# Performance work log

Measured on AMD Instinct MI355X. Metric: run time of the kernel, lower is better.

Reference implementation:

```python
import jax, jax.numpy as jnp
import numpy as np
from jax import lax

D_MODEL = 640
D_INNER = 1280
D_STATE = 34
D_CONV = 4
DT_RANK = 40  # ceil(640/16)
DT_MIN, DT_MAX = 1e-3, 1e-1
NUM_LAYERS = 8
BATCH, SEQ = 2, 2048


def setup_inputs() -> dict:
    key = jax.random.key(0)
    ks = jax.random.split(key, 8)
    hidden_states = jax.random.normal(ks[0], (BATCH, SEQ, D_MODEL), dtype=jnp.float32)
    W_in = jax.random.normal(ks[1], (2 * D_INNER, D_MODEL), dtype=jnp.float32) * 0.02
    conv_w = jax.random.normal(ks[2], (D_INNER, D_CONV), dtype=jnp.float32) * 0.2
    conv_b = jnp.zeros((D_INNER,), dtype=jnp.float32)
    W_x = jax.random.normal(ks[3], (DT_RANK + 2 * D_STATE, D_INNER), dtype=jnp.float32) * 0.02
    W_dt = jax.random.normal(ks[4], (D_INNER, DT_RANK), dtype=jnp.float32) * 0.02
    # dt bias init: inverse-softplus of dt sampled log-uniform in [dt_min, dt_max]
    u = jax.random.uniform(ks[5], (D_INNER,), dtype=jnp.float32)
    dt_vals = jnp.exp(u * (np.log(DT_MAX) - np.log(DT_MIN)) + np.log(DT_MIN))
    dt_bias = dt_vals + jnp.log(-jnp.expm1(-dt_vals))
    A_log = jnp.log(jnp.tile(jnp.arange(1, D_STATE + 1, dtype=jnp.float32)[None, :], (D_INNER, 1)))
    D_skip = jnp.ones((D_INNER,), dtype=jnp.float32)
    W_out = jax.random.normal(ks[6], (D_MODEL, D_INNER), dtype=jnp.float32) * (0.02 / np.sqrt(2.0 * NUM_LAYERS))
    return {"hidden_states": hidden_states, "W_in": W_in, "conv_w": conv_w,
            "conv_b": conv_b, "W_x": W_x, "W_dt": W_dt, "dt_bias": dt_bias,
            "A_log": A_log, "D_skip": D_skip, "W_out": W_out}


def _silu(v):
    return v * jax.nn.sigmoid(v)


def _causal_dwconv(x, w, b):
    # x: [B, Di, L], w: [Di, K] depthwise, left-pad K-1 for causality
    out = lax.conv_general_dilated(
        x, w[:, None, :], window_strides=(1,), padding=[(D_CONV - 1, 0)],
        feature_group_count=D_INNER, dimension_numbers=("NCH", "OIH", "NCH"))
    return out + b[None, :, None]


def _selective_scan(u, dt_sp, A, Bm, Cm):
    # u, dt_sp: [B, Di, L]; A: [Di, N]; Bm, Cm: [B, L, N]
    dtl = jnp.moveaxis(dt_sp, 2, 0)  # [L, B, Di]
    ul = jnp.moveaxis(u, 2, 0)       # [L, B, Di]

    def step(h, inp):
        dt_t, u_t, B_t, C_t = inp
        dA = jnp.exp(dt_t[..., None] * A)                   # [B, Di, N]
        h = dA * h + (dt_t * u_t)[..., None] * B_t[:, None, :]
        y = jnp.einsum("bdn,bn->bd", h, C_t)
        return h, y

    h0 = jnp.zeros((u.shape[0], D_INNER, D_STATE), dtype=u.dtype)
    _, ys = lax.scan(step, h0, (dtl, ul, jnp.swapaxes(Bm, 0, 1), jnp.swapaxes(Cm, 0, 1)))
    return jnp.moveaxis(ys, 0, 2)  # [B, Di, L]


def reference(hidden_states, W_in, conv_w, conv_b, W_x, W_dt, dt_bias, A_log, D_skip, W_out):
    # in_proj and split into x / gate z, channels-first
    xz = hidden_states @ W_in.T                    # [B, L, 2*Di]
    x = jnp.swapaxes(xz[..., :D_INNER], 1, 2)      # [B, Di, L]
    z = jnp.swapaxes(xz[..., D_INNER:], 1, 2)      # [B, Di, L]
    # causal depthwise conv + silu
    x = _silu(_causal_dwconv(x, conv_w, conv_b))
    # input-dependent dt, B, C
    x_dbl = jnp.swapaxes(x, 1, 2) @ W_x.T          # [B, L, dt_rank + 2N]
    dt_raw = x_dbl[..., :DT_RANK]
    Bm = x_dbl[..., DT_RANK:DT_RANK + D_STATE]     # [B, L, N]
    Cm = x_dbl[..., DT_RANK + D_STATE:]            # [B, L, N]
    dt = jnp.swapaxes(dt_raw @ W_dt.T, 1, 2)       # [B, Di, L]
    dt_sp = jax.nn.softplus(dt + dt_bias[None, :, None])
    A = -jnp.exp(A_log)                            # [Di, N]
    y = _selective_scan(x, dt_sp, A, Bm, Cm)
    y = y + x * D_skip[None, :, None]
    y = y * _silu(z)
    return jnp.swapaxes(y, 1, 2) @ W_out.T         # [B, L, d_model]
```

## Files before the change

kernel.cpp:

```cpp
#include <hip/hip_runtime.h>
#include <hip/hip_bf16.h>

#define D_MODEL   640
#define D_INNER   1280
#define D_STATE   34
#define D_CONV    4
#define DT_RANK   40
#define BATCH     2
#define SEQ       2048
#define XDBL_W    (DT_RANK + 2 * D_STATE)
#define M_TOTAL   (BATCH * SEQ)
#define NCHUNK    8
#define CHLEN     (SEQ / NCHUNK)
#define NQ        (CHLEN / 4)
#define RECW      68

typedef __attribute__((ext_vector_type(8))) short short8v;
typedef __attribute__((ext_vector_type(4))) short short4v;
typedef __attribute__((ext_vector_type(4))) float f32x4;

__device__ __forceinline__ void split_bf16(float x, short& hi, short& lo) {
    unsigned u  = __builtin_bit_cast(unsigned, x);
    unsigned uh = u & 0xFFFF0000u;
    hi = (short)(uh >> 16);
    float r = x - __builtin_bit_cast(float, uh);
    unsigned v = __builtin_bit_cast(unsigned, r);
    v += 0x7FFFu + ((v >> 16) & 1u);
    lo = (short)(v >> 16);
}

__device__ __forceinline__ void split4(const float4& v, short4v& h, short4v& l) {
    float xs[4] = {v.x, v.y, v.z, v.w};
    #pragma unroll
    for (int j = 0; j < 4; ++j) { short hh, ll; split_bf16(xs[j], hh, ll); h[j] = hh; l[j] = ll; }
}

template<int MODE>
__global__ __launch_bounds__(256) void gemm_mfma(
    const float* __restrict__ A, const float* __restrict__ B,
    float* __restrict__ C, int M, int N, int K, int lda, int ldb, int ldc)
{
    constexpr int BMt = 128, BKt = 32;
    constexpr int LDT = 40;
    __shared__ short Ahi[BMt * LDT], Alo[BMt * LDT];
    __shared__ short Bhi[BMt * LDT], Blo[BMt * LDT];

    const int tid  = threadIdx.x;
    const long m0  = (long)blockIdx.y * BMt;
    const long n0  = (long)blockIdx.x * BMt;
    const int wid  = tid >> 6, lane = tid & 63;
    const int wr   = (wid >> 1) * 64;
    const int wc   = (wid & 1) * 64;
    const int lrow = lane & 15;
    const int lkb  = lane >> 4;

    const bool do_silu = (MODE == 2) && (m0 >= D_INNER);

    f32x4 acc[4][4] = {};

    for (int k0 = 0; k0 < K; k0 += BKt) {
        __syncthreads();
        #pragma unroll
        for (int q = 0; q < 4; ++q) {
            int flat = tid + q * 256;
            int r  = flat >> 3;
            int f4 = (flat & 7) << 2;
            float4 va = *reinterpret_cast<const float4*>(&A[(m0 + r) * lda + k0 + f4]);
            float4 vb = *reinterpret_cast<const float4*>(&B[(n0 + r) * ldb + k0 + f4]);
            short4v ah, al, bh, bl;
            split4(va, ah, al);
            split4(vb, bh, bl);
            *reinterpret_cast<short4v*>(&Ahi[r * LDT + f4]) = ah;
            *reinterpret_cast<short4v*>(&Alo[r * LDT + f4]) = al;
            *reinterpret_cast<short4v*>(&Bhi[r * LDT + f4]) = bh;
            *reinterpret_cast<short4v*>(&Blo[r * LDT + f4]) = bl;
        }
        __syncthreads();

        short8v a_hi[4], a_lo[4], b_hi[4], b_lo[4];
        #pragma unroll
        for (int i = 0; i < 4; ++i) {
            int ar = (wr + i * 16 + lrow) * LDT + lkb * 8;
            int br = (wc + i * 16 + lrow) * LDT + lkb * 8;
            a_hi[i] = *reinterpret_cast<const short8v*>(&Ahi[ar]);
            a_lo[i] = *reinterpret_cast<const short8v*>(&Alo[ar]);
            b_hi[i] = *reinterpret_cast<const short8v*>(&Bhi[br]);
            b_lo[i] = *reinterpret_cast<const short8v*>(&Blo[br]);
        }
        #pragma unroll
        for (int i = 0; i < 4; ++i)
            #pragma unroll
            for (int j = 0; j < 4; ++j) {
                acc[i][j] = __builtin_amdgcn_mfma_f32_16x16x32_bf16(a_hi[i], b_hi[j], acc[i][j], 0, 0, 0);
                acc[i][j] = __builtin_amdgcn_mfma_f32_16x16x32_bf16(a_hi[i], b_lo[j], acc[i][j], 0, 0, 0);
                acc[i][j] = __builtin_amdgcn_mfma_f32_16x16x32_bf16(a_lo[i], b_hi[j], acc[i][j], 0, 0, 0);
            }
    }

    #pragma unroll
    for (int i = 0; i < 4; ++i) {
        long grow0 = m0 + wr + i * 16 + lkb * 4;
        #pragma unroll
        for (int j = 0; j < 4; ++j) {
            long gcol = n0 + wc + j * 16 + lrow;
            #pragma unroll
            for (int r = 0; r < 4; ++r) {
                float v = acc[i][j][r];
                if (do_silu) v = v * (1.0f / (1.0f + __expf(-v)));
                C[(grow0 + r) * ldc + gcol] = v;
            }
        }
    }
}

#define BM 64
#define BN 64
#define BK 16

template<int LAYA, int LAYB, int MODE>
__global__ __launch_bounds__(256) void gemm_tn(
    const float* __restrict__ A, const float* __restrict__ B,
    float* __restrict__ C, int M, int N, int K, int lda, int ldb, int ldc,
    const float* __restrict__ bias)
{
    __shared__ float As[BK][BM + 4];
    __shared__ float Bs[BK][BN + 4];

    const int tid = threadIdx.x;
    const int m0 = blockIdx.y * BM;
    const int n0 = blockIdx.x * BN;
    const int tx = tid & 15;
    const int ty = tid >> 4;

    float acc[4][4] = {};

    for (int k0 = 0; k0 < K; k0 += BK) {
        #pragma unroll
        for (int i = 0; i < 4; ++i) {
            int idx = tid + i * 256;
            if (LAYA == 0) {
                int r = idx >> 4;
                int c = idx & 15;
                As[c][r] = (m0 + r < M && k0 + c < K)
                         ? A[(long)(m0 + r) * lda + (k0 + c)] : 0.0f;
            } else {
                int c = idx >> 6;
                int r = idx & 63;
                As[c][r] = (m0 + r < M && k0 + c < K)
                         ? A[(long)(k0 + c) * lda + (m0 + r)] : 0.0f;
            }
            if (LAYB == 0) {
                int rb = idx >> 4;
                int cb = idx & 15;
                Bs[cb][rb] = (n0 + rb < N && k0 + cb < K)
                           ? B[(long)(n0 + rb) * ldb + (k0 + cb)] : 0.0f;
            } else {
                int cb = idx >> 6;
                int rb = idx & 63;
                Bs[cb][rb] = (n0 + rb < N && k0 + cb < K)
                           ? B[(long)(k0 + cb) * ldb + (n0 + rb)] : 0.0f;
            }
        }
        __syncthreads();

        #pragma unroll
        for (int k = 0; k < BK; ++k) {
            const float4 a4 = *reinterpret_cast<const float4*>(&As[k][ty * 4]);
            const float4 b4 = *reinterpret_cast<const float4*>(&Bs[k][tx * 4]);
            const float a_[4] = {a4.x, a4.y, a4.z, a4.w};
            const float b_[4] = {b4.x, b4.y, b4.z, b4.w};
            #pragma unroll
            for (int i = 0; i < 4; ++i)
                #pragma unroll
                for (int j = 0; j < 4; ++j)
                    acc[i][j] = fmaf(a_[i], b_[j], acc[i][j]);
        }
        __syncthreads();
    }

    #pragma unroll
    for (int i = 0; i < 4; ++i) {
        int gm = m0 + ty * 4 + i;
        if (gm >= M) continue;
        float bi = (MODE == 2) ? bias[gm] : 0.0f;
        #pragma unroll
        for (int j = 0; j < 4; ++j) {
            int gn = n0 + tx * 4 + j;
            if (gn >= N) continue;
            float v = acc[i][j];
            if (MODE == 2) {
                v += bi;
                v = (v > 15.0f) ? v : log1pf(__expf(v));
            }
            C[(long)gm * ldc + gn] = v;
        }
    }
}

__global__ __launch_bounds__(256) void gemm_splitk_T(
    const float* __restrict__ A, const float* __restrict__ B,
    float* __restrict__ Cp, int M, int N, int K, int lda, int ldb, int ldc)
{
    __shared__ float As[BK][BM + 4];
    __shared__ float Bs[BK][BN + 4];

    const int tid = threadIdx.x;
    const int m0 = blockIdx.y * BM;
    const int n0 = blockIdx.x * BN;
    const int z  = blockIdx.z;
    const int kseg = K / 4;
    const int kbeg = z * kseg;
    const int tx = tid & 15;
    const int ty = tid >> 4;

    float acc[4][4] = {};

    for (int k0 = kbeg; k0 < kbeg + kseg; k0 += BK) {
        #pragma unroll
        for (int i = 0; i < 4; ++i) {
            int idx = tid + i * 256;
            int r = idx >> 4;
            int c = idx & 15;
            As[c][r] = (m0 + r < M) ? A[(long)(m0 + r) * lda + (k0 + c)] : 0.0f;
            int cb = idx >> 6;
            int rb = idx & 63;
            Bs[cb][rb] = B[(long)(k0 + cb) * ldb + (n0 + rb)];
        }
        __syncthreads();

        #pragma unroll
        for (int k = 0; k < BK; ++k) {
            const float4 a4 = *reinterpret_cast<const float4*>(&As[k][ty * 4]);
            const float4 b4 = *reinterpret_cast<const float4*>(&Bs[k][tx * 4]);
            const float a_[4] = {a4.x, a4.y, a4.z, a4.w};
            const float b_[4] = {b4.x, b4.y, b4.z, b4.w};
            #pragma unroll
            for (int i = 0; i < 4; ++i)
                #pragma unroll
                for (int j = 0; j < 4; ++j)
                    acc[i][j] = fmaf(a_[i], b_[j], acc[i][j]);
        }
        __syncthreads();
    }

    float* Cz = Cp + (long)z * M * ldc;
    #pragma unroll
    for (int i = 0; i < 4; ++i) {
        int gm = m0 + ty * 4 + i;
        if (gm >= M) continue;
        #pragma unroll
        for (int j = 0; j < 4; ++j) {
            int gn = n0 + tx * 4 + j;
            Cz[(long)gm * ldc + gn] = acc[i][j];
        }
    }
}

__global__ __launch_bounds__(256) void reduce4_kernel(
    const float* __restrict__ part, float* __restrict__ out, int n)
{
    int i4 = (blockIdx.x * 256 + threadIdx.x) * 4;
    if (i4 >= n) return;
    float4 s0 = *reinterpret_cast<const float4*>(&part[i4]);
    float4 s1 = *reinterpret_cast<const float4*>(&part[(long)n + i4]);
    float4 s2 = *reinterpret_cast<const float4*>(&part[(long)2 * n + i4]);
    float4 s3 = *reinterpret_cast<const float4*>(&part[(long)3 * n + i4]);
    float4 r;
    r.x = (s0.x + s1.x) + (s2.x + s3.x);
    r.y = (s0.y + s1.y) + (s2.y + s3.y);
    r.z = (s0.z + s1.z) + (s2.z + s3.z);
    r.w = (s0.w + s1.w) + (s2.w + s3.w);
    *reinterpret_cast<float4*>(&out[i4]) = r;
}

__global__ __launch_bounds__(256) void conv_silu_kernel(
    const float* __restrict__ xT, const float* __restrict__ cw,
    const float* __restrict__ cb, float* __restrict__ uT)
{
    int idx = blockIdx.x * 256 + threadIdx.x;
    if (idx >= D_INNER * M_TOTAL) return;
    int bs = idx & (M_TOTAL - 1);
    int d  = idx >> 12;
    int s  = bs & (SEQ - 1);

    const float* xr = xT + idx;
    float acc = cb[d];
    #pragma unroll
    for (int k = 0; k < D_CONV; ++k) {
        int off = k - (D_CONV - 1);
        if (s + off >= 0)
            acc = fmaf(xr[off], cw[d * D_CONV + k], acc);
    }
    uT[idx] = acc * (1.0f / (1.0f + __expf(-acc)));
}

__global__ __launch_bounds__(256) void transpose_kernel(
    const float* __restrict__ in, float* __restrict__ out)
{
    __shared__ float tile[32][33];
    const int tx = threadIdx.x & 31;
    const int ty = threadIdx.x >> 5;
    const int t0 = blockIdx.x * 32;
    const int d0 = blockIdx.y * 32;

    #pragma unroll
    for (int i = 0; i < 32; i += 8)
        tile[ty + i][tx] = in[(long)(d0 + ty + i) * M_TOTAL + t0 + tx];
    __syncthreads();
    #pragma unroll
    for (int i = 0; i < 32; i += 8)
        out[(long)(t0 + ty + i) * D_INNER + d0 + tx] = tile[tx][ty + i];
}

#define DPP_ADD(X_, CTRL_) {                                                 \
        int t_ = __builtin_amdgcn_update_dpp(                                \
            0, __builtin_bit_cast(int, X_), (CTRL_), 0xf, 0xf, true);        \
        X_ += __builtin_bit_cast(float, t_);                                 \
    }

__global__ __launch_bounds__(64) void scan_part1(
    const float* __restrict__ xdblT,
    const float* __restrict__ spT,
    const float* __restrict__ A_log,
    const float* __restrict__ uT,
    float* __restrict__ rec)
{
    const int cid  = blockIdx.x;
    const int bd   = cid / (NCHUNK - 1);
    const int c    = cid % (NCHUNK - 1);
    const int lane = threadIdx.x;
    const int b = bd / D_INNER;
    const int d = bd % D_INNER;
    const bool act = lane < D_STATE;

    const float A_n = act ? -__expf(A_log[d * D_STATE + lane]) : 0.0f;

    const long tbase = (long)b * SEQ + (long)c * CHLEN;
    const float* sp_p = spT + (long)d * M_TOTAL + tbase;
    const float* u_p  = uT  + (long)d * M_TOTAL + tbase;
    const float* Bp   = xdblT + (long)(act ? DT_RANK + lane : 0) * M_TOTAL + tbase;

    float h = 0.0f, P = 1.0f;

    float4 aSP, aU, aB, bSP, bU, bB;

#define LOADQ1(SP_, U_, B_, Q_) {                                            \
        int qq = (Q_); qq = (qq < NQ) ? qq : (NQ - 1); int tt = qq * 4;      \
        SP_ = *reinterpret_cast<const float4*>(&sp_p[tt]);                   \
        U_  = *reinterpret_cast<const float4*>(&u_p[tt]);                    \
        B_  = *reinterpret_cast<const float4*>(&Bp[tt]);                     \
        if (!act) B_ = make_float4(0.f, 0.f, 0.f, 0.f);                      \
    }

#define ST1(SPX, UX, BX) {                                                   \
        float dA = __expf((SPX) * A_n);                                      \
        h = fmaf(dA, h, ((SPX) * (UX)) * (BX));                              \
        P *= dA;                                                             \
    }

#define STEPQ1(SP_, U_, B_) {                                                \
        ST1(SP_.x, U_.x, B_.x); ST1(SP_.y, U_.y, B_.y);                      \
        ST1(SP_.z, U_.z, B_.z); ST1(SP_.w, U_.w, B_.w);                      \
    }

    LOADQ1(aSP, aU, aB, 0);
    for (int q = 0; q < NQ; q += 2) {
        LOADQ1(bSP, bU, bB, q + 1);
        STEPQ1(aSP, aU, aB);
        LOADQ1(aSP, aU, aB, q + 2);
        STEPQ1(bSP, bU, bB);
    }
#undef LOADQ1
#undef ST1
#undef STEPQ1

    if (act) {
        rec[(long)cid * RECW + lane]      = h;
        rec[(long)cid * RECW + 34 + lane] = P;
    }
}

__global__ __launch_bounds__(64) void scan_part3(
    const float* __restrict__ gT,
    const float* __restrict__ xdblT,
    const float* __restrict__ spT,
    const float* __restrict__ A_log,
    const float* __restrict__ D_skip,
    const float* __restrict__ rec,
    float* __restrict__ uT)
{
    const int cid  = blockIdx.x;
    const int bd   = cid >> 3;
    const int c    = cid & (NCHUNK - 1);
    const int lane = threadIdx.x;
    const int b = bd / D_INNER;
    const int d = bd % D_INNER;
    const bool act = lane < D_STATE;

    const float A_n = act ? -__expf(A_log[d * D_STATE + lane]) : 0.0f;
    const float Dd  = D_skip[d];

    const long tbase = (long)b * SEQ + (long)c * CHLEN;
    const float* sp_p = spT + (long)d * M_TOTAL + tbase;
    const float* g_p  = gT  + (long)d * M_TOTAL + tbase;
    float*       u_p  = uT  + (long)d * M_TOTAL + tbase;
    const float* Bp   = xdblT + (long)(act ? DT_RANK + lane : 0) * M_TOTAL + tbase;
    const float* Cp   = xdblT + (long)(act ? DT_RANK + D_STATE + lane : 0) * M_TOTAL + tbase;

    float h = 0.0f;
    for (int cc = 0; cc < c; ++cc) {
        long rbase = (long)(bd * (NCHUNK - 1) + cc) * RECW;
        float he = act ? rec[rbase + lane]      : 0.0f;
        float Pp = act ? rec[rbase + 34 + lane] : 0.0f;
        h = fmaf(Pp, h, he);
    }

    float4 aSP, aU, aG, aB, aC, bSP, bU, bG, bB, bC;

#define LOADQ(SP_, U_, G_, B_, C_, Q_) {                                     \
        int qq = (Q_); qq = (qq < NQ) ? qq : (NQ - 1); int tt = qq * 4;      \
        SP_ = *reinterpret_cast<const float4*>(&sp_p[tt]);                   \
        U_  = *reinterpret_cast<const float4*>(&u_p[tt]);                    \
        G_  = *reinterpret_cast<const float4*>(&g_p[tt]);                    \
        B_  = *reinterpret_cast<const float4*>(&Bp[tt]);                     \
        C_  = *reinterpret_cast<const float4*>(&Cp[tt]);                     \
        if (!act) { B_ = make_float4(0.f,0.f,0.f,0.f);                       \
                    C_ = make_float4(0.f,0.f,0.f,0.f); }                     \
    }

#define ST(SPX, UX, GX, BX, CX, YX) {                                        \
        float dA = __expf((SPX) * A_n);                                      \
        h = fmaf(dA, h, ((SPX) * (UX)) * (BX));                              \
        float pp = h * (CX);                                                 \
        DPP_ADD(pp, 0x111);                                  \
        DPP_ADD(pp, 0x112);                                  \
        DPP_ADD(pp, 0x114);                                  \
        DPP_ADD(pp, 0x118);                                  \
        DPP_ADD(pp, 0x142);                                \
        DPP_ADD(pp, 0x143);                                \
        YX = fmaf((UX), Dd, pp) * (GX);                                      \
    }

#define STEPQ(SP_, U_, G_, B_, C_, Q_) {                                     \
        float4 yq;                                                           \
        ST(SP_.x, U_.x, G_.x, B_.x, C_.x, yq.x);                             \
        ST(SP_.y, U_.y, G_.y, B_.y, C_.y, yq.y);                             \
        ST(SP_.z, U_.z, G_.z, B_.z, C_.z, yq.z);                             \
        ST(SP_.w, U_.w, G_.w, B_.w, C_.w, yq.w);                             \
        if (lane == 63)                                                      \
            *reinterpret_cast<float4*>(&u_p[(Q_) * 4]) = yq;                 \
    }

    LOADQ(aSP, aU, aG, aB, aC, 0);
    for (int q = 0; q < NQ; q += 2) {
        LOADQ(bSP, bU, bG, bB, bC, q + 1);
        STEPQ(aSP, aU, aG, aB, aC, q);
        LOADQ(aSP, aU, aG, aB, aC, q + 2);
        STEPQ(bSP, bU, bG, bB, bC, q + 1);
    }
#undef LOADQ
#undef ST
#undef STEPQ
}

extern "C" void kernel_launch(void* const* d_in, const int* in_sizes, int n_in,
                              void* d_out, int out_size, void* d_ws, size_t ws_size,
                              hipStream_t stream)
{
    const float* hs      = (const float*)d_in[0];
    const float* W_in    = (const float*)d_in[1];
    const float* conv_w  = (const float*)d_in[2];
    const float* conv_b  = (const float*)d_in[3];
    const float* W_x     = (const float*)d_in[4];
    const float* W_dt    = (const float*)d_in[5];
    const float* dt_bias = (const float*)d_in[6];
    const float* A_log   = (const float*)d_in[7];
    const float* D_skip  = (const float*)d_in[8];
    const float* W_out   = (const float*)d_in[9];
    float* out = (float*)d_out;

    float* ws    = (float*)d_ws;
    float* xT    = ws;
    float* gT    = xT    + (size_t)D_INNER * M_TOTAL;
    float* uT    = gT    + (size_t)D_INNER * M_TOTAL;
    float* xdblT = uT    + (size_t)D_INNER * M_TOTAL;
    float* spT   = xdblT + (size_t)XDBL_W * M_TOTAL;
    float* rec   = spT   + (size_t)D_INNER * M_TOTAL;
    float* part  = xT;
    float* yN    = xT;

    dim3 blk(256);

    gemm_mfma<2><<<dim3(M_TOTAL / 128, (2 * D_INNER) / 128), blk, 0, stream>>>(
        W_in, hs, xT, 2 * D_INNER, M_TOTAL, D_MODEL, D_MODEL, D_MODEL, M_TOTAL);

    conv_silu_kernel<<<(D_INNER * M_TOTAL + 255) / 256, blk, 0, stream>>>(
        xT, conv_w, conv_b, uT);

    gemm_splitk_T<<<dim3(M_TOTAL / BN, (XDBL_W + BM - 1) / BM, 4), blk, 0, stream>>>(
        W_x, uT, part, XDBL_W, M_TOTAL, D_INNER, D_INNER, M_TOTAL, M_TOTAL);

    reduce4_kernel<<<(XDBL_W * M_TOTAL / 4 + 255) / 256, blk, 0, stream>>>(
        part, xdblT, XDBL_W * M_TOTAL);

    gemm_tn<0, 1, 2><<<dim3(M_TOTAL / BN, D_INNER / BM), blk, 0, stream>>>(
        W_dt, xdblT, spT, D_INNER, M_TOTAL, DT_RANK, DT_RANK, M_TOTAL, M_TOTAL,
        dt_bias);

    scan_part1<<<BATCH * D_INNER * (NCHUNK - 1), 64, 0, stream>>>(
        xdblT, spT, A_log, uT, rec);

    scan_part3<<<BATCH * D_INNER * NCHUNK, 64, 0, stream>>>(
        gT, xdblT, spT, A_log, D_skip, rec, uT);

    transpose_kernel<<<dim3(M_TOTAL / 32, D_INNER / 32), blk, 0, stream>>>(uT, yN);

    gemm_mfma<0><<<dim3(D_MODEL / 128, M_TOTAL / 128), blk, 0, stream>>>(
        yN, W_out, out, M_TOTAL, D_MODEL, D_INNER, D_INNER, D_INNER, D_MODEL);
}
```

Before: 629.9 us.

## Halve scan chunk count and batch-load four quads per scan iteration

Cuts the number of sequence chunks in the chunked selective scan from 8 to 4, so each block walks a longer chunk and there are fewer inter-chunk carry records to combine. The double-buffered load/step macros are replaced by a loop that issues loads for four float4 quads up front and then processes them, aiming for more memory-level parallelism per wave. Launch bounds now request 4 waves per SIMD to cap register use. The risk is fewer blocks (less parallelism) and longer serial chains per block, and the larger register arrays may cause spills under the tighter bound.

```diff
diff --git a/kernel.cpp b/kernel.cpp
--- a/kernel.cpp
+++ b/kernel.cpp
@@ -10,9 +10,10 @@
 #define SEQ       2048
 #define XDBL_W    (DT_RANK + 2 * D_STATE)
 #define M_TOTAL   (BATCH * SEQ)
-#define NCHUNK    8
+#define NCHUNK    4
 #define CHLEN     (SEQ / NCHUNK)
 #define NQ        (CHLEN / 4)
+#define QB        4
 #define RECW      68
 
 typedef __attribute__((ext_vector_type(8))) short short8v;
@@ -318,7 +319,7 @@
         X_ += __builtin_bit_cast(float, t_);                                 \
     }
 
-__global__ __launch_bounds__(64) void scan_part1(
+__global__ __launch_bounds__(64, 4) void scan_part1(
     const float* __restrict__ xdblT,
     const float* __restrict__ spT,
     const float* __restrict__ A_log,
@@ -342,37 +343,32 @@
 
     float h = 0.0f, P = 1.0f;
 
-    float4 aSP, aU, aB, bSP, bU, bB;
-
-#define LOADQ1(SP_, U_, B_, Q_) {                                            \
-        int qq = (Q_); qq = (qq < NQ) ? qq : (NQ - 1); int tt = qq * 4;      \
-        SP_ = *reinterpret_cast<const float4*>(&sp_p[tt]);                   \
-        U_  = *reinterpret_cast<const float4*>(&u_p[tt]);                    \
-        B_  = *reinterpret_cast<const float4*>(&Bp[tt]);                     \
-        if (!act) B_ = make_float4(0.f, 0.f, 0.f, 0.f);                      \
-    }
-
 #define ST1(SPX, UX, BX) {                                                   \
         float dA = __expf((SPX) * A_n);                                      \
         h = fmaf(dA, h, ((SPX) * (UX)) * (BX));                              \
         P *= dA;                                                             \
     }
 
-#define STEPQ1(SP_, U_, B_) {                                                \
-        ST1(SP_.x, U_.x, B_.x); ST1(SP_.y, U_.y, B_.y);                      \
-        ST1(SP_.z, U_.z, B_.z); ST1(SP_.w, U_.w, B_.w);                      \
-    }
-
-    LOADQ1(aSP, aU, aB, 0);
-    for (int q = 0; q < NQ; q += 2) {
-        LOADQ1(bSP, bU, bB, q + 1);
-        STEPQ1(aSP, aU, aB);
-        LOADQ1(aSP, aU, aB, q + 2);
-        STEPQ1(bSP, bU, bB);
-    }
-#undef LOADQ1
+    #pragma unroll 1
+    for (int q0 = 0; q0 < NQ; q0 += QB) {
+        float4 SP[QB], U[QB], Bq[QB];
+        #pragma unroll
+        for (int i = 0; i < QB; ++i) {
+            int tt = (q0 + i) * 4;
+            SP[i] = *reinterpret_cast<const float4*>(&sp_p[tt]);
+            U[i]  = *reinterpret_cast<const float4*>(&u_p[tt]);
+            Bq[i] = *reinterpret_cast<const float4*>(&Bp[tt]);
+            if (!act) Bq[i] = make_float4(0.f, 0.f, 0.f, 0.f);
+        }
+        #pragma unroll
+        for (int i = 0; i < QB; ++i) {
+            ST1(SP[i].x, U[i].x, Bq[i].x);
+            ST1(SP[i].y, U[i].y, Bq[i].y);
+            ST1(SP[i].z, U[i].z, Bq[i].z);
+            ST1(SP[i].w, U[i].w, Bq[i].w);
+        }
+    }
 #undef ST1
-#undef STEPQ1
 
     if (act) {
         rec[(long)cid * RECW + lane]      = h;
@@ -380,7 +376,7 @@
     }
 }
 
-__global__ __launch_bounds__(64) void scan_part3(
+__global__ __launch_bounds__(64, 4) void scan_part3(
     const float* __restrict__ gT,
     const float* __restrict__ xdblT,
     const float* __restrict__ spT,
@@ -390,7 +386,7 @@
     float* __restrict__ uT)
 {
     const int cid  = blockIdx.x;
-    const int bd   = cid >> 3;
+    const int bd   = cid >> 2;
     const int c    = cid & (NCHUNK - 1);
     const int lane = threadIdx.x;
     const int b = bd / D_INNER;
@@ -413,19 +409,6 @@
         float he = act ? rec[rbase + lane]      : 0.0f;
         float Pp = act ? rec[rbase + 34 + lane] : 0.0f;
         h = fmaf(Pp, h, he);
-    }
-
-    float4 aSP, aU, aG, aB, aC, bSP, bU, bG, bB, bC;
-
-#define LOADQ(SP_, U_, G_, B_, C_, Q_) {                                     \
-        int qq = (Q_); qq = (qq < NQ) ? qq : (NQ - 1); int tt = qq * 4;      \
-        SP_ = *reinterpret_cast<const float4*>(&sp_p[tt]);                   \
-        U_  = *reinterpret_cast<const float4*>(&u_p[tt]);                    \
-        G_  = *reinterpret_cast<const float4*>(&g_p[tt]);                    \
-        B_  = *reinterpret_cast<const float4*>(&Bp[tt]);                     \
-        C_  = *reinterpret_cast<const float4*>(&Cp[tt]);                     \
-        if (!act) { B_ = make_float4(0.f,0.f,0.f,0.f);                       \
-                    C_ = make_float4(0.f,0.f,0.f,0.f); }                     \
     }
 
 #define ST(SPX, UX, GX, BX, CX, YX) {                                        \
@@ -441,26 +424,32 @@
         YX = fmaf((UX), Dd, pp) * (GX);                                      \
     }
 
-#define STEPQ(SP_, U_, G_, B_, C_, Q_) {                                     \
-        float4 yq;                                                           \
-        ST(SP_.x, U_.x, G_.x, B_.x, C_.x, yq.x);                             \
-        ST(SP_.y, U_.y, G_.y, B_.y, C_.y, yq.y);                             \
-        ST(SP_.z, U_.z, G_.z, B_.z, C_.z, yq.z);                             \
-        ST(SP_.w, U_.w, G_.w, B_.w, C_.w, yq.w);                             \
-        if (lane == 63)                                                      \
-            *reinterpret_cast<float4*>(&u_p[(Q_) * 4]) = yq;                 \
-    }
-
-    LOADQ(aSP, aU, aG, aB, aC, 0);
-    for (int q = 0; q < NQ; q += 2) {
-        LOADQ(bSP, bU, bG, bB, bC, q + 1);
-        STEPQ(aSP, aU, aG, aB, aC, q);
-        LOADQ(aSP, aU, aG, aB, aC, q + 2);
-        STEPQ(bSP, bU, bG, bB, bC, q + 1);
-    }
-#undef LOADQ
+    #pragma unroll 1
+    for (int q0 = 0; q0 < NQ; q0 += QB) {
+        float4 SP[QB], U[QB], G[QB], Bq[QB], Cq[QB];
+        #pragma unroll
+        for (int i = 0; i < QB; ++i) {
+            int tt = (q0 + i) * 4;
+            SP[i] = *reinterpret_cast<const float4*>(&sp_p[tt]);
+            U[i]  = *reinterpret_cast<const float4*>(&u_p[tt]);
+            G[i]  = *reinterpret_cast<const float4*>(&g_p[tt]);
+            Bq[i] = *reinterpret_cast<const float4*>(&Bp[tt]);
+            Cq[i] = *reinterpret_cast<const float4*>(&Cp[tt]);
+            if (!act) { Bq[i] = make_float4(0.f,0.f,0.f,0.f);
+                        Cq[i] = make_float4(0.f,0.f,0.f,0.f); }
+        }
+        #pragma unroll
+        for (int i = 0; i < QB; ++i) {
+            float4 yq;
+            ST(SP[i].x, U[i].x, G[i].x, Bq[i].x, Cq[i].x, yq.x);
+            ST(SP[i].y, U[i].y, G[i].y, Bq[i].y, Cq[i].y, yq.y);
+            ST(SP[i].z, U[i].z, G[i].z, Bq[i].z, Cq[i].z, yq.z);
+            ST(SP[i].w, U[i].w, G[i].w, Bq[i].w, Cq[i].w, yq.w);
+            if (lane == 63)
+                *reinterpret_cast<float4*>(&u_p[(q0 + i) * 4]) = yq;
+        }
+    }
 #undef ST
-#undef STEPQ
 }
 
 extern "C" void kernel_launch(void* const* d_in, const int* in_sizes, int n_in,
```

Result: faster. 584.3 us (-7.2%).
